# Kernel tuning notes

Measured on AMD Instinct MI355X. Metric: run time of the kernel, lower is better.

## Reference

```python
import jax, jax.numpy as jnp
import numpy as np

B, S, D = 1, 2048, 1024
NH, NKV, WS = 8, 2, 64
HD = D // NH  # 128
E, HDIM, TOPK = 16, 512, 2
FP16_MIN = -65504.0
EPS = 1e-6
AUX_COEFF = 1e-5


def rmsnorm(x, w):
    return x * jax.lax.rsqrt(jnp.mean(x * x, axis=-1, keepdims=True) + EPS) * w


def setup_inputs() -> dict:
    key = jax.random.key(0)
    ks = jax.random.split(key, 24)
    r = lambda k, shape, fan: jax.random.normal(k, shape, dtype=jnp.float32) * (1.0 / np.sqrt(fan))
    return {
        "x": jax.random.normal(ks[0], (B, S, D), dtype=jnp.float32),
        "norm1_w": jnp.ones((D,), jnp.float32),
        "wq": r(ks[1], (D, NH * HD), D), "bq": jnp.zeros((NH * HD,), jnp.float32),
        "wk": r(ks[2], (D, NKV * HD), D), "bk": jnp.zeros((NKV * HD,), jnp.float32),
        "wv": r(ks[3], (D, NKV * HD), D), "bv": jnp.zeros((NKV * HD,), jnp.float32),
        "wo": r(ks[4], (NH * HD, D), NH * HD), "bo": jnp.zeros((D,), jnp.float32),
        "sink_bias": jnp.zeros((), jnp.float32),
        "norm2_w": jnp.ones((D,), jnp.float32),
        "router_w": r(ks[5], (D, E), D), "router_b": jnp.zeros((E,), jnp.float32),
        "w1": r(ks[6], (E, D, HDIM), D), "b1": jnp.zeros((E, HDIM), jnp.float32),
        "w2": r(ks[7], (E, HDIM, D), HDIM), "b2": jnp.zeros((E, D), jnp.float32),
    }


def reference(x, norm1_w, wq, bq, wk, bk, wv, bv, wo, bo, sink_bias,
              norm2_w, router_w, router_b, w1, b1, w2, b2):
    # ---- sliding-window attention with sink softmax ----
    h = rmsnorm(x, norm1_w)
    q = (h @ wq + bq).reshape(B, S, NH, HD).transpose(0, 2, 1, 3)    # [B,NH,S,HD]
    k = (h @ wk + bk).reshape(B, S, NKV, HD).transpose(0, 2, 1, 3)   # [B,NKV,S,HD]
    v = (h @ wv + bv).reshape(B, S, NKV, HD).transpose(0, 2, 1, 3)
    k = jnp.repeat(k, NH // NKV, axis=1)  # GQA expand -> [B,NH,S,HD]
    v = jnp.repeat(v, NH // NKV, axis=1)
    scores = jnp.einsum('bhqd,bhkd->bhqk', q, k) / np.sqrt(HD)
    i = jnp.arange(S)[:, None]
    j = jnp.arange(S)[None, :]
    band = (i - j >= 0) & (i - j <= WS - 1)  # causal sliding window
    scores = jnp.where(band, scores, FP16_MIN)
    m = jnp.maximum(jnp.max(scores, axis=-1, keepdims=True), sink_bias)
    ew = jnp.exp(scores - m)
    denom = jnp.sum(ew, axis=-1, keepdims=True) + jnp.exp(sink_bias - m)
    attn = ew / denom
    out = jnp.einsum('bhqk,bhkd->bhqd', attn, v).transpose(0, 2, 1, 3).reshape(B, S, D)
    x = x + (out @ wo + bo)

    # ---- MoE FFN ----
    h2 = rmsnorm(x, norm2_w)
    xf = h2.reshape(-1, D)                                  # [N,D]
    logits = (xf @ router_w + router_b) / 0.1               # [N,E]
    top_v, top_i = jax.lax.top_k(logits, TOPK)              # [N,k]
    top_w = jax.nn.softmax(top_v, axis=-1)
    probs = jax.nn.softmax(logits, axis=-1)
    aux_loss = jnp.sum(jnp.sum(probs, axis=0) ** 2) / E * AUX_COEFF
    # combine weights per (token, expert)
    gate = jnp.sum(jax.nn.one_hot(top_i, E, dtype=xf.dtype) * top_w[..., None], axis=1)  # [N,E]
    hmid = jax.nn.silu(jnp.einsum('nd,edh->neh', xf, w1) + b1)   # [N,E,H]
    y = jnp.einsum('neh,ehd->ned', hmid, w2) + b2                # [N,E,D]
    ffn = jnp.einsum('ne,ned->nd', gate, y)
    x = x + ffn.reshape(B, S, D)
    return x, aux_loss
```

## Files before the change

### kernel.cpp

```cpp
#include <hip/hip_runtime.h>
#include <hip/hip_bf16.h>

#define S     2048
#define D     1024
#define NH    8
#define NKV   2
#define HD    128
#define WS_   64
#define E_    16
#define HDIM  512
#define TOPK  2
#define NTOK  S
#define NSLOT (S*TOPK)
#define QKV_M (D + 2*NKV*HD)
#define KOFF  D
#define VOFF  (D + NKV*HD)
#define QB    8
#define WROWS (QB + WS_ - 1)
#define KPITCH 73
#define VPADF  132

typedef __attribute__((ext_vector_type(8))) short bf16x8;
typedef __attribute__((ext_vector_type(4))) float floatx4;

__device__ inline short f2bf(float f) {
    __hip_bfloat16 b = __float2bfloat16(f);
    return *reinterpret_cast<short*>(&b);
}

__global__ __launch_bounds__(256) void tconv_all(
    const float* __restrict__ wq, const float* __restrict__ wk,
    const float* __restrict__ wv, const float* __restrict__ wo,
    const float* __restrict__ w1, const float* __restrict__ w2,
    const float* __restrict__ bq, const float* __restrict__ bk,
    const float* __restrict__ bv, const float* __restrict__ router_w,
    short* __restrict__ wqkvT, short* __restrict__ woT,
    short* __restrict__ w1T, short* __restrict__ w2T,
    float* __restrict__ bqkv, float* __restrict__ rwT)
{
    int id = blockIdx.x;
    if (id >= 18950) {
        int ky = id - 18950;
        int t = threadIdx.x;
        int r = t >> 4, c = t & 15;
        int k0 = ky * 32;
        rwT[c * D + k0 + r]      = router_w[(k0 + r) * E_ + c];
        rwT[c * D + k0 + r + 16] = router_w[(k0 + r + 16) * E_ + c];
        return;
    }
    if (id >= 18944) {
        int t = (id - 18944) * 256 + threadIdx.x;
        if (t < D) bqkv[t] = bq[t];
        else if (t < VOFF) bqkv[t] = bk[t - D];
        else bqkv[t] = bv[t - VOFF];
        return;
    }
    const float* in; short* outp; int K, M, mx, ky;
    if (id < 1024)      { in = wq; outp = wqkvT;                  K = D; M = D;   int l = id;        mx = l & 31; ky = l >> 5; }
    else if (id < 1280) { in = wk; outp = wqkvT + (size_t)KOFF*D; K = D; M = 256; int l = id - 1024; mx = l & 7;  ky = l >> 3; }
    else if (id < 1536) { in = wv; outp = wqkvT + (size_t)VOFF*D; K = D; M = 256; int l = id - 1280; mx = l & 7;  ky = l >> 3; }
    else if (id < 2560) { in = wo; outp = woT;                    K = D; M = D;   int l = id - 1536; mx = l & 31; ky = l >> 5; }
    else if (id < 10752){ int l = id - 2560;  int e = l >> 9; int r = l & 511;
                          in = w1 + (size_t)e * D * HDIM; outp = w1T + (size_t)e * D * HDIM;
                          K = D; M = HDIM; mx = r & 15; ky = r >> 4; }
    else                { int l = id - 10752; int e = l >> 9; int r = l & 511;
                          in = w2 + (size_t)e * D * HDIM; outp = w2T + (size_t)e * D * HDIM;
                          K = HDIM; M = D; mx = r & 31; ky = r >> 5; }
    __shared__ float tile[32][33];
    int t = threadIdx.x, r = t >> 3, c4 = (t & 7) * 4;
    int k0 = ky * 32, m0 = mx * 32;
    float4 v = *(const float4*)&in[(size_t)(k0 + r) * M + m0 + c4];
    tile[r][c4 + 0] = v.x; tile[r][c4 + 1] = v.y;
    tile[r][c4 + 2] = v.z; tile[r][c4 + 3] = v.w;
    __syncthreads();
    short4 o;
    o.x = f2bf(tile[c4 + 0][r]);
    o.y = f2bf(tile[c4 + 1][r]);
    o.z = f2bf(tile[c4 + 2][r]);
    o.w = f2bf(tile[c4 + 3][r]);
    *(short4*)&outp[(size_t)(m0 + r) * K + k0 + c4] = o;
}

__global__ __launch_bounds__(256) void rmsnorm_kernel(
    const float* __restrict__ x, const float* __restrict__ w,
    short* __restrict__ outb)
{
    int row = blockIdx.x, t = threadIdx.x;
    float4 v = ((const float4*)(x + (size_t)row * D))[t];
    float ss = v.x*v.x + v.y*v.y + v.z*v.z + v.w*v.w;
    #pragma unroll
    for (int off = 32; off; off >>= 1) ss += __shfl_xor(ss, off, 64);
    __shared__ float red[4];
    if ((t & 63) == 0) red[t >> 6] = ss;
    __syncthreads();
    float total = red[0] + red[1] + red[2] + red[3];
    float scale = rsqrtf(total * (1.0f / (float)D) + 1e-6f);
    float4 wv = ((const float4*)w)[t];
    short4 ob;
    ob.x = f2bf(v.x * scale * wv.x); ob.y = f2bf(v.y * scale * wv.y);
    ob.z = f2bf(v.z * scale * wv.z); ob.w = f2bf(v.w * scale * wv.w);
    ((short4*)(outb + (size_t)row * D))[t] = ob;
}

#define BT   64
#define BKS  64
#define BUFS (BT * BKS)

__device__ inline void gld16(const short* g, short* l) {
    __builtin_amdgcn_global_load_lds(
        (const __attribute__((address_space(1))) unsigned int*)g,
        (__attribute__((address_space(3))) unsigned int*)l, 16, 0, 0);
}

template <int V>
__global__ __launch_bounds__(256) void mgemm(
    const short* __restrict__ A, const short* __restrict__ Bt,
    const float* __restrict__ bias, float* __restrict__ C,
    short* __restrict__ Cb, const float* __restrict__ res, int K, int M,
    const int* __restrict__ offs, const float* __restrict__ tok_gate)
{
    int e = (V >= 2) ? blockIdx.z : 0;
    const short* Bte = (V >= 2) ? Bt + (size_t)e * M * K : Bt;
    const float* be  = (V >= 2) ? bias + (size_t)e * M : bias;

    int row_lo, row_hi;
    if (V >= 2) {
        row_lo = offs[e] + blockIdx.y * BT;
        row_hi = offs[e + 1];
        if (row_lo >= row_hi) return;
    } else {
        row_lo = blockIdx.y * BT;
        row_hi = 1 << 30;
    }
    int col0 = blockIdx.x * BT;

    __shared__ __align__(16) short As[2 * BUFS];
    __shared__ __align__(16) short Bs[2 * BUFS];

    int t = threadIdx.x;
    int wave = t >> 6, lane = t & 63;
    int lrow   = lane >> 3;
    int schunk = (lane & 7) ^ lrow;

    const short* aQ[2];
    const short* bQ[2];
    #pragma unroll
    for (int q = 0; q < 2; ++q) {
        int row = q * 32 + wave * 8 + lrow;
        int gr = row_lo + row;
        if (V >= 2 && gr >= row_hi) gr = row_lo;
        aQ[q] = A   + (size_t)gr * K + (schunk << 3);
        bQ[q] = Bte + (size_t)(col0 + row) * K + (schunk << 3);
    }

    int rin = lane & 15, quad = lane >> 4;
    int wm = (wave & 1) * 32, wn = (wave >> 1) * 32;

    floatx4 acc[2][2];
    #pragma unroll
    for (int i = 0; i < 2; ++i)
        #pragma unroll
        for (int j = 0; j < 2; ++j)
            acc[i][j] = (floatx4){0.f, 0.f, 0.f, 0.f};

    const int NIT = K >> 6;

    #pragma unroll
    for (int q = 0; q < 2; ++q) {
        gld16(aQ[q], &As[(q * 32 + wave * 8) * BKS]);
        gld16(bQ[q], &Bs[(q * 32 + wave * 8) * BKS]);
    }
    __syncthreads();

    for (int it = 0; it < NIT; ++it) {
        int cur = it & 1, nxt = cur ^ 1;
        if (it + 1 < NIT) {
            int kk = (it + 1) << 6;
            #pragma unroll
            for (int q = 0; q < 2; ++q) {
                gld16(aQ[q] + kk, &As[nxt * BUFS + (q * 32 + wave * 8) * BKS]);
                gld16(bQ[q] + kk, &Bs[nxt * BUFS + (q * 32 + wave * 8) * BKS]);
            }
        }
        const short* Ab = &As[cur * BUFS];
        const short* Bb = &Bs[cur * BUFS];
        #pragma unroll
        for (int s = 0; s < 2; ++s) {
            bf16x8 af[2], bfr[2];
            #pragma unroll
            for (int i = 0; i < 2; ++i) {
                int row = wm + i * 16 + rin;
                af[i] = *(const bf16x8*)&Ab[row * BKS
                        + ((((s << 2) | quad) ^ (rin & 7)) << 3)];
            }
            #pragma unroll
            for (int j = 0; j < 2; ++j) {
                int row = wn + j * 16 + rin;
                bfr[j] = *(const bf16x8*)&Bb[row * BKS
                        + ((((s << 2) | quad) ^ (rin & 7)) << 3)];
            }
            #pragma unroll
            for (int i = 0; i < 2; ++i)
                #pragma unroll
                for (int j = 0; j < 2; ++j)
                    acc[i][j] = __builtin_amdgcn_mfma_f32_16x16x32_bf16(
                        af[i], bfr[j], acc[i][j], 0, 0, 0);
        }
        __syncthreads();
    }

    #pragma unroll
    for (int i = 0; i < 2; ++i) {
        #pragma unroll
        for (int j = 0; j < 2; ++j) {
            int cg = col0 + wn + j * 16 + rin;
            #pragma unroll
            for (int rr = 0; rr < 4; ++rr) {
                int rg = row_lo + wm + i * 16 + quad * 4 + rr;
                float val = acc[i][j][rr];
                if (V == 0) {
                    C[(size_t)rg * M + cg] = val + be[cg];
                } else if (V == 1) {
                    C[(size_t)rg * M + cg] = val + be[cg] + res[(size_t)rg * M + cg];
                } else if (V == 2) {
                    if (rg < row_hi) {
                        float vb_ = val + be[cg];
                        Cb[(size_t)rg * M + cg] = f2bf(vb_ / (1.f + __expf(-vb_)));
                    }
                } else {
                    if (rg < row_hi)
                        C[(size_t)rg * M + cg] = tok_gate[rg] * (val + be[cg]);
                }
            }
        }
    }
}

__global__ __launch_bounds__(256) void attn_kernel(
    const float* __restrict__ qkv, const float* __restrict__ sink_ptr,
    short* __restrict__ ao)
{
    __shared__ __align__(16) float KT[32 * KPITCH * 4];
    __shared__ __align__(16) float Vs[WROWS * VPADF];
    __shared__ __align__(16) float Ps4[4][64][4];

    int qblk = blockIdx.x;
    int kvh  = blockIdx.y;
    int q0   = qblk * QB;
    int jbase = q0 - (WS_ - 1);

    int t = threadIdx.x;
    int c4 = (t & 31) * 4, c4g = t & 31;
    for (int r = t >> 5; r < WROWS; r += 8) {
        int j = jbase + r;
        float4 kv4 = make_float4(0.f, 0.f, 0.f, 0.f);
        float4 vv4 = make_float4(0.f, 0.f, 0.f, 0.f);
        if (j >= 0) {
            kv4 = *(const float4*)(qkv + (size_t)j * QKV_M + KOFF + kvh * HD + c4);
            vv4 = *(const float4*)(qkv + (size_t)j * QKV_M + VOFF + kvh * HD + c4);
        }
        *(float4*)&KT[(c4g * KPITCH + r) * 4] = kv4;
        *(float4*)&Vs[r * VPADF + c4] = vv4;
    }
    __syncthreads();

    int lane = t & 63, wv = t >> 6;
    float sink = sink_ptr[0];
    const float rscale = 0.08838834764831845f;

    #pragma unroll
    for (int g = 0; g < 2; ++g) {
        int qi = wv * 2 + g;
        int i  = q0 + qi;
        bool valid = (jbase + qi + lane) >= 0;

        float sc[4] = {0.f, 0.f, 0.f, 0.f};
        const float* qbase = qkv + (size_t)i * QKV_M + (kvh * 4) * HD;
        #pragma unroll
        for (int c = 0; c < 32; ++c) {
            float4 kx = *(const float4*)&KT[(c * KPITCH + qi + lane) * 4];
            #pragma unroll
            for (int hh = 0; hh < 4; ++hh) {
                float4 q4 = *(const float4*)(qbase + hh * HD + c * 4);
                sc[hh] += q4.x*kx.x + q4.y*kx.y + q4.z*kx.z + q4.w*kx.w;
            }
        }

        float pn[4];
        #pragma unroll
        for (int hh = 0; hh < 4; ++hh) {
            float s = valid ? sc[hh] * rscale : -1e30f;
            float m = s;
            #pragma unroll
            for (int off = 32; off; off >>= 1) m = fmaxf(m, __shfl_xor(m, off, 64));
            float mf = fmaxf(m, sink);
            float p  = __expf(s - mf);
            float ds = p;
            #pragma unroll
            for (int off = 32; off; off >>= 1) ds += __shfl_xor(ds, off, 64);
            pn[hh] = p / (ds + __expf(sink - mf));
        }
        *(float4*)&Ps4[wv][lane][0] = make_float4(pn[0], pn[1], pn[2], pn[3]);

        float o0=0,o1=0,o2=0,o3=0,o4=0,o5=0,o6=0,o7=0;
        const float* vp = &Vs[qi * VPADF + 2 * lane];
        #pragma unroll
        for (int jj = 0; jj < 64; ++jj) {
            float4 p4 = *(const float4*)&Ps4[wv][jj][0];
            float2 vv = *(const float2*)(vp + jj * VPADF);
            o0 += p4.x * vv.x; o1 += p4.x * vv.y;
            o2 += p4.y * vv.x; o3 += p4.y * vv.y;
            o4 += p4.z * vv.x; o5 += p4.z * vv.y;
            o6 += p4.w * vv.x; o7 += p4.w * vv.y;
        }
        short2 r0; r0.x = f2bf(o0); r0.y = f2bf(o1);
        short2 r1; r1.x = f2bf(o2); r1.y = f2bf(o3);
        short2 r2; r2.x = f2bf(o4); r2.y = f2bf(o5);
        short2 r3; r3.x = f2bf(o6); r3.y = f2bf(o7);
        ((short2*)(ao + (size_t)i * D + (kvh * 4 + 0) * HD))[lane] = r0;
        ((short2*)(ao + (size_t)i * D + (kvh * 4 + 1) * HD))[lane] = r1;
        ((short2*)(ao + (size_t)i * D + (kvh * 4 + 2) * HD))[lane] = r2;
        ((short2*)(ao + (size_t)i * D + (kvh * 4 + 3) * HD))[lane] = r3;
    }
}

__global__ __launch_bounds__(256) void rms_router_kernel(
    const float* __restrict__ x1, const float* __restrict__ w,
    short* __restrict__ h2b, const float* __restrict__ rwT,
    const float* __restrict__ rb, float* __restrict__ probs,
    int* __restrict__ top_i, float* __restrict__ top_g)
{
    int tok = blockIdx.x, t = threadIdx.x;
    __shared__ float hrow[D];
    float4 v = ((const float4*)(x1 + (size_t)tok * D))[t];
    float ss = v.x*v.x + v.y*v.y + v.z*v.z + v.w*v.w;
    #pragma unroll
    for (int off = 32; off; off >>= 1) ss += __shfl_xor(ss, off, 64);
    __shared__ float red[4];
    if ((t & 63) == 0) red[t >> 6] = ss;
    __syncthreads();
    float total = red[0] + red[1] + red[2] + red[3];
    float scale = rsqrtf(total * (1.0f / (float)D) + 1e-6f);
    float4 wv = ((const float4*)w)[t];
    float4 o;
    o.x = v.x * scale * wv.x; o.y = v.y * scale * wv.y;
    o.z = v.z * scale * wv.z; o.w = v.w * scale * wv.w;
    ((float4*)hrow)[t] = o;
    short4 ob;
    ob.x = f2bf(o.x); ob.y = f2bf(o.y); ob.z = f2bf(o.z); ob.w = f2bf(o.w);
    ((short4*)(h2b + (size_t)tok * D))[t] = ob;
    __syncthreads();

    int e = t & 15, seg = t >> 4;
    const float4* rwp = (const float4*)(rwT + (size_t)e * D + seg * 64);
    const float4* hp  = (const float4*)(hrow + seg * 64);
    float part = 0.f;
    #pragma unroll
    for (int i = 0; i < 16; ++i) {
        float4 a = hp[i];
        float4 b = rwp[i];
        part += a.x * b.x; part += a.y * b.y;
        part += a.z * b.z; part += a.w * b.w;
    }
    __shared__ float lpart[256];
    lpart[t] = part;
    __syncthreads();
    __shared__ float logits[E_];
    if (t < E_) {
        float sl = 0.f;
        for (int sg = 0; sg < 16; ++sg) sl += lpart[sg * 16 + t];
        logits[t] = (sl + rb[t]) * 10.0f;
    }
    __syncthreads();
    __shared__ float sm[2];
    if (t == 0) {
        float mx = logits[0];
        for (int x = 1; x < E_; ++x) mx = fmaxf(mx, logits[x]);
        float ps = 0.f;
        for (int x = 0; x < E_; ++x) ps += __expf(logits[x] - mx);
        sm[0] = mx; sm[1] = ps;
        int i0 = 0; float v0 = logits[0];
        for (int x = 1; x < E_; ++x) if (logits[x] > v0) { v0 = logits[x]; i0 = x; }
        int i1 = (i0 == 0) ? 1 : 0; float v1 = logits[i1];
        for (int x = 0; x < E_; ++x) {
            if (x == i0) continue;
            if (logits[x] > v1) { v1 = logits[x]; i1 = x; }
        }
        float e1 = __expf(v1 - v0);
        float g0 = 1.f / (1.f + e1);
        float g1 = e1 * g0;
        top_i[tok * 2 + 0] = i0; top_g[tok * 2 + 0] = g0;
        top_i[tok * 2 + 1] = i1; top_g[tok * 2 + 1] = g1;
    }
    __syncthreads();
    if (t < E_) probs[tok * E_ + t] = __expf(logits[t] - sm[0]) / sm[1];
}

__global__ __launch_bounds__(256) void finalize_kernel(
    const float* __restrict__ probs, const int* __restrict__ top_i,
    int* __restrict__ offs, int* __restrict__ cursor,
    float* __restrict__ aux_out)
{
    __shared__ float csum[E_];
    __shared__ int hist[E_];
    int t = threadIdx.x;
    if (t < E_) { csum[t] = 0.f; hist[t] = 0; }
    __syncthreads();

    int c = t & 15, g = t >> 4;
    float part = 0.f;
    for (int i = 0; i < NTOK / 16; ++i)
        part += probs[(size_t)(i * 16 + g) * E_ + c];
    atomicAdd(&csum[c], part);

    for (int i = 0; i < NSLOT / 256; ++i) {
        int eidx = top_i[i * 256 + t] & 15;
        atomicAdd(&hist[eidx], 1);
    }
    __syncthreads();

    if (t == 0) {
        int acc = 0;
        for (int e = 0; e < E_; ++e) { offs[e] = acc; cursor[e] = acc; acc += hist[e]; }
        offs[E_] = acc;
        float s = 0.f;
        for (int e = 0; e < E_; ++e) s += csum[e] * csum[e];
        *aux_out = s / (float)E_ * 1e-5f;
    }
}

__global__ __launch_bounds__(256) void scatter_kernel(
    const int* __restrict__ top_i, const float* __restrict__ top_g,
    int* __restrict__ cursor, int* __restrict__ tok_idx,
    float* __restrict__ tok_gate, int* __restrict__ slot_of)
{
    int tok = blockIdx.x * 256 + threadIdx.x;
    if (tok >= NTOK) return;
    for (int s = 0; s < TOPK; ++s) {
        int e = top_i[tok * 2 + s] & 15;
        int pos = atomicAdd(&cursor[e], 1) & (NSLOT - 1);
        tok_idx[pos]  = tok;
        tok_gate[pos] = top_g[tok * 2 + s];
        slot_of[tok * 2 + s] = pos;
    }
}

__global__ __launch_bounds__(256) void gather_kernel(
    const short* __restrict__ h2b, const int* __restrict__ tok_idx,
    short* __restrict__ xg)
{
    int slot = blockIdx.x * 2 + (threadIdx.x >> 7);
    int c = (threadIdx.x & 127) * 8;
    int tok = tok_idx[slot] & (NTOK - 1);
    *(float4*)&xg[(size_t)slot * D + c] =
        *(const float4*)&h2b[(size_t)tok * D + c];
}

__global__ __launch_bounds__(256) void combine_kernel(
    const float* __restrict__ x1, const float* __restrict__ y,
    const int* __restrict__ slot_of, float* __restrict__ out)
{
    int tok = blockIdx.x, t = threadIdx.x;
    int s0 = slot_of[tok * 2] & (NSLOT - 1), s1 = slot_of[tok * 2 + 1] & (NSLOT - 1);
    float4 a = ((const float4*)(x1 + (size_t)tok * D))[t];
    float4 b = ((const float4*)(y + (size_t)s0 * D))[t];
    float4 c = ((const float4*)(y + (size_t)s1 * D))[t];
    float4 o;
    o.x = a.x + b.x + c.x; o.y = a.y + b.y + c.y;
    o.z = a.z + b.z + c.z; o.w = a.w + b.w + c.w;
    ((float4*)(out + (size_t)tok * D))[t] = o;
}

extern "C" void kernel_launch(void* const* d_in, const int* in_sizes, int n_in,
                              void* d_out, int out_size, void* d_ws, size_t ws_size,
                              hipStream_t stream)
{
    const float* x        = (const float*)d_in[0];
    const float* norm1_w  = (const float*)d_in[1];
    const float* wq       = (const float*)d_in[2];
    const float* bq       = (const float*)d_in[3];
    const float* wk       = (const float*)d_in[4];
    const float* bk       = (const float*)d_in[5];
    const float* wv       = (const float*)d_in[6];
    const float* bv       = (const float*)d_in[7];
    const float* wo       = (const float*)d_in[8];
    const float* bo       = (const float*)d_in[9];
    const float* sink     = (const float*)d_in[10];
    const float* norm2_w  = (const float*)d_in[11];
    const float* router_w = (const float*)d_in[12];
    const float* router_b = (const float*)d_in[13];
    const float* w1       = (const float*)d_in[14];
    const float* b1       = (const float*)d_in[15];
    const float* w2       = (const float*)d_in[16];
    const float* b2       = (const float*)d_in[17];
    float* out = (float*)d_out;

    char* w = (char*)d_ws;
    auto alloc = [&](size_t bytes) {
        char* p = w; w += (bytes + 255) & ~255ull; return p;
    };
    short* wqkvT = (short*)alloc((size_t)QKV_M * D * 2);
    short* woT   = (short*)alloc((size_t)D * D * 2);
    short* w1T   = (short*)alloc((size_t)E_ * HDIM * D * 2);
    short* w2T   = (short*)alloc((size_t)E_ * D * HDIM * 2);
    float* bqkv  = (float*)alloc(QKV_M * 4);
    float* rwT   = (float*)alloc((size_t)E_ * D * 4);
    short* h_bf  = (short*)alloc((size_t)S * D * 2);
    float* qkv   = (float*)alloc((size_t)S * QKV_M * 4);
    float* x1    = (float*)alloc((size_t)S * D * 4);
    short* h2b   = (short*)alloc((size_t)S * D * 2);
    short* xg    = (short*)alloc((size_t)NSLOT * D * 2);
    float* yslot = (float*)alloc((size_t)NSLOT * D * 4);
    float* probs = (float*)alloc((size_t)NTOK * E_ * 4);
    int*   offs     = (int*)alloc(17 * 4);
    int*   cursor   = (int*)alloc(16 * 4);
    int*   top_i    = (int*)alloc((size_t)NSLOT * 4);
    float* top_g    = (float*)alloc((size_t)NSLOT * 4);
    int*   tok_idx  = (int*)alloc((size_t)NSLOT * 4);
    float* tok_gate = (float*)alloc((size_t)NSLOT * 4);
    int*   slot_of  = (int*)alloc((size_t)NSLOT * 4);
    short* ao_bf = h_bf;
    short* hmid  = (short*)qkv;

    tconv_all<<<18982, 256, 0, stream>>>(wq, wk, wv, wo, w1, w2, bq, bk, bv,
                                         router_w, wqkvT, woT, w1T, w2T,
                                         bqkv, rwT);

    rmsnorm_kernel<<<S, 256, 0, stream>>>(x, norm1_w, h_bf);

    mgemm<0><<<dim3(QKV_M / BT, S / BT), 256, 0, stream>>>(
        h_bf, wqkvT, bqkv, qkv, nullptr, nullptr, D, QKV_M, nullptr, nullptr);

    attn_kernel<<<dim3(S / QB, NKV), 256, 0, stream>>>(qkv, sink, ao_bf);

    mgemm<1><<<dim3(D / BT, S / BT), 256, 0, stream>>>(
        ao_bf, woT, bo, x1, nullptr, x, D, D, nullptr, nullptr);

    rms_router_kernel<<<NTOK, 256, 0, stream>>>(x1, norm2_w, h2b, rwT,
                                                router_b, probs, top_i, top_g);

    finalize_kernel<<<1, 256, 0, stream>>>(probs, top_i, offs, cursor,
                                           out + (size_t)S * D);

    scatter_kernel<<<(NTOK + 255) / 256, 256, 0, stream>>>(
        top_i, top_g, cursor, tok_idx, tok_gate, slot_of);

    gather_kernel<<<NSLOT / 2, 256, 0, stream>>>(h2b, tok_idx, xg);

    mgemm<2><<<dim3(HDIM / BT, NSLOT / BT, E_), 256, 0, stream>>>(
        xg, w1T, b1, nullptr, hmid, nullptr, D, HDIM, offs, nullptr);

    mgemm<3><<<dim3(D / BT, NSLOT / BT, E_), 256, 0, stream>>>(
        hmid, w2T, b2, yslot, nullptr, nullptr, HDIM, D, offs, tok_gate);

    combine_kernel<<<NTOK, 256, 0, stream>>>(x1, yslot, slot_of, out);
}
```

Before: 296.6 us.

## Fuse MoE gather/combine into expert GEMMs and merge small launches

The first rmsnorm now runs as extra blocks inside the weight-conversion kernel. Finalize and scatter are merged into one single-block kernel. The gather kernel is dropped: the first expert GEMM reads token rows indirectly through tok_idx. The combine kernel is also dropped: the router kernel writes x1 into out, and the second expert GEMM atomically adds gated results into out. This removes four kernel launches and the xg/yslot intermediate buffers. In exchange, float atomics make the summation order nondeterministic, and the scatter now runs serially on one block.

```diff
diff --git a/kernel.cpp b/kernel.cpp
--- a/kernel.cpp
+++ b/kernel.cpp
@@ -36,9 +36,29 @@
     const float* __restrict__ bv, const float* __restrict__ router_w,
     short* __restrict__ wqkvT, short* __restrict__ woT,
     short* __restrict__ w1T, short* __restrict__ w2T,
-    float* __restrict__ bqkv, float* __restrict__ rwT)
+    float* __restrict__ bqkv, float* __restrict__ rwT,
+    const float* __restrict__ x, const float* __restrict__ norm1_w,
+    short* __restrict__ h_bf)
 {
     int id = blockIdx.x;
+    if (id >= 18982) {
+        int row = id - 18982, t = threadIdx.x;
+        float4 v = ((const float4*)(x + (size_t)row * D))[t];
+        float ss = v.x*v.x + v.y*v.y + v.z*v.z + v.w*v.w;
+        #pragma unroll
+        for (int off = 32; off; off >>= 1) ss += __shfl_xor(ss, off, 64);
+        __shared__ float red[4];
+        if ((t & 63) == 0) red[t >> 6] = ss;
+        __syncthreads();
+        float total = red[0] + red[1] + red[2] + red[3];
+        float scale = rsqrtf(total * (1.0f / (float)D) + 1e-6f);
+        float4 wv4 = ((const float4*)norm1_w)[t];
+        short4 ob;
+        ob.x = f2bf(v.x * scale * wv4.x); ob.y = f2bf(v.y * scale * wv4.y);
+        ob.z = f2bf(v.z * scale * wv4.z); ob.w = f2bf(v.w * scale * wv4.w);
+        ((short4*)(h_bf + (size_t)row * D))[t] = ob;
+        return;
+    }
     if (id >= 18950) {
         int ky = id - 18950;
         int t = threadIdx.x;
@@ -81,27 +101,6 @@
     *(short4*)&outp[(size_t)(m0 + r) * K + k0 + c4] = o;
 }
 
-__global__ __launch_bounds__(256) void rmsnorm_kernel(
-    const float* __restrict__ x, const float* __restrict__ w,
-    short* __restrict__ outb)
-{
-    int row = blockIdx.x, t = threadIdx.x;
-    float4 v = ((const float4*)(x + (size_t)row * D))[t];
-    float ss = v.x*v.x + v.y*v.y + v.z*v.z + v.w*v.w;
-    #pragma unroll
-    for (int off = 32; off; off >>= 1) ss += __shfl_xor(ss, off, 64);
-    __shared__ float red[4];
-    if ((t & 63) == 0) red[t >> 6] = ss;
-    __syncthreads();
-    float total = red[0] + red[1] + red[2] + red[3];
-    float scale = rsqrtf(total * (1.0f / (float)D) + 1e-6f);
-    float4 wv = ((const float4*)w)[t];
-    short4 ob;
-    ob.x = f2bf(v.x * scale * wv.x); ob.y = f2bf(v.y * scale * wv.y);
-    ob.z = f2bf(v.z * scale * wv.z); ob.w = f2bf(v.w * scale * wv.w);
-    ((short4*)(outb + (size_t)row * D))[t] = ob;
-}
-
 #define BT   64
 #define BKS  64
 #define BUFS (BT * BKS)
@@ -117,7 +116,8 @@
     const short* __restrict__ A, const short* __restrict__ Bt,
     const float* __restrict__ bias, float* __restrict__ C,
     short* __restrict__ Cb, const float* __restrict__ res, int K, int M,
-    const int* __restrict__ offs, const float* __restrict__ tok_gate)
+    const int* __restrict__ offs, const float* __restrict__ tok_gate,
+    const int* __restrict__ tok_map)
 {
     int e = (V >= 2) ? blockIdx.z : 0;
     const short* Bte = (V >= 2) ? Bt + (size_t)e * M * K : Bt;
@@ -149,7 +149,10 @@
         int row = q * 32 + wave * 8 + lrow;
         int gr = row_lo + row;
         if (V >= 2 && gr >= row_hi) gr = row_lo;
-        aQ[q] = A   + (size_t)gr * K + (schunk << 3);
+        const short* arow;
+        if (V == 2) arow = A + (size_t)(tok_map[gr] & (NTOK - 1)) * K;
+        else        arow = A + (size_t)gr * K;
+        aQ[q] = arow + (schunk << 3);
         bQ[q] = Bte + (size_t)(col0 + row) * K + (schunk << 3);
     }
 
@@ -228,8 +231,11 @@
                         Cb[(size_t)rg * M + cg] = f2bf(vb_ / (1.f + __expf(-vb_)));
                     }
                 } else {
-                    if (rg < row_hi)
-                        C[(size_t)rg * M + cg] = tok_gate[rg] * (val + be[cg]);
+                    if (rg < row_hi) {
+                        int tok = tok_map[rg] & (NTOK - 1);
+                        unsafeAtomicAdd(&C[(size_t)tok * M + cg],
+                                        tok_gate[rg] * (val + be[cg]));
+                    }
                 }
             }
         }
@@ -328,11 +334,13 @@
     const float* __restrict__ x1, const float* __restrict__ w,
     short* __restrict__ h2b, const float* __restrict__ rwT,
     const float* __restrict__ rb, float* __restrict__ probs,
-    int* __restrict__ top_i, float* __restrict__ top_g)
+    int* __restrict__ top_i, float* __restrict__ top_g,
+    float* __restrict__ out)
 {
     int tok = blockIdx.x, t = threadIdx.x;
     __shared__ float hrow[D];
     float4 v = ((const float4*)(x1 + (size_t)tok * D))[t];
+    ((float4*)(out + (size_t)tok * D))[t] = v;
     float ss = v.x*v.x + v.y*v.y + v.z*v.z + v.w*v.w;
     #pragma unroll
     for (int off = 32; off; off >>= 1) ss += __shfl_xor(ss, off, 64);
@@ -375,16 +383,16 @@
     __shared__ float sm[2];
     if (t == 0) {
         float mx = logits[0];
-        for (int x = 1; x < E_; ++x) mx = fmaxf(mx, logits[x]);
+        for (int x_ = 1; x_ < E_; ++x_) mx = fmaxf(mx, logits[x_]);
         float ps = 0.f;
-        for (int x = 0; x < E_; ++x) ps += __expf(logits[x] - mx);
+        for (int x_ = 0; x_ < E_; ++x_) ps += __expf(logits[x_] - mx);
         sm[0] = mx; sm[1] = ps;
         int i0 = 0; float v0 = logits[0];
-        for (int x = 1; x < E_; ++x) if (logits[x] > v0) { v0 = logits[x]; i0 = x; }
+        for (int x_ = 1; x_ < E_; ++x_) if (logits[x_] > v0) { v0 = logits[x_]; i0 = x_; }
         int i1 = (i0 == 0) ? 1 : 0; float v1 = logits[i1];
-        for (int x = 0; x < E_; ++x) {
-            if (x == i0) continue;
-            if (logits[x] > v1) { v1 = logits[x]; i1 = x; }
+        for (int x_ = 0; x_ < E_; ++x_) {
+            if (x_ == i0) continue;
+            if (logits[x_] > v1) { v1 = logits[x_]; i1 = x_; }
         }
         float e1 = __expf(v1 - v0);
         float g0 = 1.f / (1.f + e1);
@@ -396,13 +404,15 @@
     if (t < E_) probs[tok * E_ + t] = __expf(logits[t] - sm[0]) / sm[1];
 }
 
-__global__ __launch_bounds__(256) void finalize_kernel(
+__global__ __launch_bounds__(256) void finalize_scatter_kernel(
     const float* __restrict__ probs, const int* __restrict__ top_i,
-    int* __restrict__ offs, int* __restrict__ cursor,
-    float* __restrict__ aux_out)
+    const float* __restrict__ top_g, int* __restrict__ offs,
+    int* __restrict__ tok_idx, float* __restrict__ tok_gate,
+    int* __restrict__ slot_of, float* __restrict__ aux_out)
 {
     __shared__ float csum[E_];
     __shared__ int hist[E_];
+    __shared__ int curs[E_];
     int t = threadIdx.x;
     if (t < E_) { csum[t] = 0.f; hist[t] = 0; }
     __syncthreads();
@@ -421,54 +431,25 @@
 
     if (t == 0) {
         int acc = 0;
-        for (int e = 0; e < E_; ++e) { offs[e] = acc; cursor[e] = acc; acc += hist[e]; }
+        for (int e = 0; e < E_; ++e) { offs[e] = acc; curs[e] = acc; acc += hist[e]; }
         offs[E_] = acc;
         float s = 0.f;
         for (int e = 0; e < E_; ++e) s += csum[e] * csum[e];
         *aux_out = s / (float)E_ * 1e-5f;
     }
-}
-
-__global__ __launch_bounds__(256) void scatter_kernel(
-    const int* __restrict__ top_i, const float* __restrict__ top_g,
-    int* __restrict__ cursor, int* __restrict__ tok_idx,
-    float* __restrict__ tok_gate, int* __restrict__ slot_of)
-{
-    int tok = blockIdx.x * 256 + threadIdx.x;
-    if (tok >= NTOK) return;
-    for (int s = 0; s < TOPK; ++s) {
-        int e = top_i[tok * 2 + s] & 15;
-        int pos = atomicAdd(&cursor[e], 1) & (NSLOT - 1);
-        tok_idx[pos]  = tok;
-        tok_gate[pos] = top_g[tok * 2 + s];
-        slot_of[tok * 2 + s] = pos;
-    }
-}
-
-__global__ __launch_bounds__(256) void gather_kernel(
-    const short* __restrict__ h2b, const int* __restrict__ tok_idx,
-    short* __restrict__ xg)
-{
-    int slot = blockIdx.x * 2 + (threadIdx.x >> 7);
-    int c = (threadIdx.x & 127) * 8;
-    int tok = tok_idx[slot] & (NTOK - 1);
-    *(float4*)&xg[(size_t)slot * D + c] =
-        *(const float4*)&h2b[(size_t)tok * D + c];
-}
-
-__global__ __launch_bounds__(256) void combine_kernel(
-    const float* __restrict__ x1, const float* __restrict__ y,
-    const int* __restrict__ slot_of, float* __restrict__ out)
-{
-    int tok = blockIdx.x, t = threadIdx.x;
-    int s0 = slot_of[tok * 2] & (NSLOT - 1), s1 = slot_of[tok * 2 + 1] & (NSLOT - 1);
-    float4 a = ((const float4*)(x1 + (size_t)tok * D))[t];
-    float4 b = ((const float4*)(y + (size_t)s0 * D))[t];
-    float4 c = ((const float4*)(y + (size_t)s1 * D))[t];
-    float4 o;
-    o.x = a.x + b.x + c.x; o.y = a.y + b.y + c.y;
-    o.z = a.z + b.z + c.z; o.w = a.w + b.w + c.w;
-    ((float4*)(out + (size_t)tok * D))[t] = o;
+    __syncthreads();
+
+    for (int i = 0; i < NTOK / 256; ++i) {
+        int tok = i * 256 + t;
+        #pragma unroll
+        for (int s = 0; s < TOPK; ++s) {
+            int e = top_i[tok * 2 + s] & 15;
+            int pos = atomicAdd(&curs[e], 1) & (NSLOT - 1);
+            tok_idx[pos]  = tok;
+            tok_gate[pos] = top_g[tok * 2 + s];
+            slot_of[tok * 2 + s] = pos;
+        }
+    }
 }
 
 extern "C" void kernel_launch(void* const* d_in, const int* in_sizes, int n_in,
@@ -509,11 +490,8 @@
     float* qkv   = (float*)alloc((size_t)S * QKV_M * 4);
     float* x1    = (float*)alloc((size_t)S * D * 4);
     short* h2b   = (short*)alloc((size_t)S * D * 2);
-    short* xg    = (short*)alloc((size_t)NSLOT * D * 2);
-    float* yslot = (float*)alloc((size_t)NSLOT * D * 4);
     float* probs = (float*)alloc((size_t)NTOK * E_ * 4);
     int*   offs     = (int*)alloc(17 * 4);
-    int*   cursor   = (int*)alloc(16 * 4);
     int*   top_i    = (int*)alloc((size_t)NSLOT * 4);
     float* top_g    = (float*)alloc((size_t)NSLOT * 4);
     int*   tok_idx  = (int*)alloc((size_t)NSLOT * 4);
@@ -522,36 +500,30 @@
     short* ao_bf = h_bf;
     short* hmid  = (short*)qkv;
 
-    tconv_all<<<18982, 256, 0, stream>>>(wq, wk, wv, wo, w1, w2, bq, bk, bv,
+    tconv_all<<<21030, 256, 0, stream>>>(wq, wk, wv, wo, w1, w2, bq, bk, bv,
                                          router_w, wqkvT, woT, w1T, w2T,
-                                         bqkv, rwT);
-
-    rmsnorm_kernel<<<S, 256, 0, stream>>>(x, norm1_w, h_bf);
+                                         bqkv, rwT, x, norm1_w, h_bf);
 
     mgemm<0><<<dim3(QKV_M / BT, S / BT), 256, 0, stream>>>(
-        h_bf, wqkvT, bqkv, qkv, nullptr, nullptr, D, QKV_M, nullptr, nullptr);
+        h_bf, wqkvT, bqkv, qkv, nullptr, nullptr, D, QKV_M, nullptr, nullptr,
+        nullptr);
 
     attn_kernel<<<dim3(S / QB, NKV), 256, 0, stream>>>(qkv, sink, ao_bf);
 
     mgemm<1><<<dim3(D / BT, S / BT), 256, 0, stream>>>(
-        ao_bf, woT, bo, x1, nullptr, x, D, D, nullptr, nullptr);
+        ao_bf, woT, bo, x1, nullptr, x, D, D, nullptr, nullptr, nullptr);
 
     rms_router_kernel<<<NTOK, 256, 0, stream>>>(x1, norm2_w, h2b, rwT,
-                                                router_b, probs, top_i, top_g);
-
-    finalize_kernel<<<1, 256, 0, stream>>>(probs, top_i, offs, cursor,
-                                           out + (size_t)S * D);
-
-    scatter_kernel<<<(NTOK + 255) / 256, 256, 0, stream>>>(
-        top_i, top_g, cursor, tok_idx, tok_gate, slot_of);
-
-    gather_kernel<<<NSLOT / 2, 256, 0, stream>>>(h2b, tok_idx, xg);
+                                                router_b, probs, top_i, top_g,
+                                                out);
+
+    finalize_scatter_kernel<<<1, 256, 0, stream>>>(
+        probs, top_i, top_g, offs, tok_idx, tok_gate, slot_of,
+        out + (size_t)S * D);
 
     mgemm<2><<<dim3(HDIM / BT, NSLOT / BT, E_), 256, 0, stream>>>(
-        xg, w1T, b1, nullptr, hmid, nullptr, D, HDIM, offs, nullptr);
+        h2b, w1T, b1, nullptr, hmid, nullptr, D, HDIM, offs, nullptr, tok_idx);
 
     mgemm<3><<<dim3(D / BT, NSLOT / BT, E_), 256, 0, stream>>>(
-        hmid, w2T, b2, yslot, nullptr, nullptr, HDIM, D, offs, tok_gate);
-
-    combine_kernel<<<NTOK, 256, 0, stream>>>(x1, yslot, slot_of, out);
-}
+        hmid, w2T, b2, out, nullptr, nullptr, HDIM, D, offs, tok_gate, tok_idx);
+}
```

After: 285.0 us. 1.04x faster.
